# Performance work log

Measured on AMD Instinct MI355X. Metric: run time of the kernel, lower is better.

Reference implementation:

```python
import jax, jax.numpy as jnp
import numpy as np

EMBED_DIM = 1024
NUM_HEADS = 16
HEAD_DIM = EMBED_DIM // NUM_HEADS
SEG_LEN = 1024  # all segment_lengths equal, dilation_rate == 1


def setup_inputs() -> dict:
    key = jax.random.key(0)
    k1, k2, k3 = jax.random.split(key, 3)
    B, S, E = 2, 4096, EMBED_DIM
    x = jax.random.normal(k1, (B, S, E), dtype=jnp.float32)
    w_qkv = jax.random.normal(k2, (3 * E, E), dtype=jnp.float32) * (E ** -0.5)
    b_qkv = jnp.zeros((3 * E,), dtype=jnp.float32)
    w_out = jax.random.normal(k3, (E, E), dtype=jnp.float32) * (E ** -0.5)
    b_out = jnp.zeros((E,), dtype=jnp.float32)
    return {"x": x, "w_qkv": w_qkv, "b_qkv": b_qkv, "w_out": w_out, "b_out": b_out}


def reference(x, w_qkv, b_qkv, w_out, b_out):
    B, S, E = x.shape
    H, Dh = NUM_HEADS, HEAD_DIM
    scale = 1.0 / np.sqrt(Dh).astype(np.float32)
    # QKV projection
    qkv = x @ w_qkv.T + b_qkv                      # [B, S, 3E]
    qkv = qkv.reshape(B, S, 3, H, Dh).transpose(2, 0, 3, 1, 4)  # [3, B, H, S, Dh]
    q, k, v = qkv[0], qkv[1], qkv[2]
    # Segments tile the sequence; each query attends only within its segment
    # (block-diagonal attention; online-softmax combine across segments is
    # trivial since the segments are disjoint in the query dimension).
    n = S // SEG_LEN
    q = q.reshape(B, H, n, SEG_LEN, Dh)
    k = k.reshape(B, H, n, SEG_LEN, Dh)
    v = v.reshape(B, H, n, SEG_LEN, Dh)
    scores = jnp.einsum("bhnqd,bhnkd->bhnqk", q, k) * scale
    attn = jax.nn.softmax(scores, axis=-1)
    out = jnp.einsum("bhnqk,bhnkd->bhnqd", attn, v)  # [B, H, n, seg, Dh]
    out = out.reshape(B, H, S, Dh).transpose(0, 2, 1, 3).reshape(B, S, E)
    return out @ w_out.T + b_out
```

## Files before the change

kernel.cpp:

```cpp
#include <hip/hip_runtime.h>

typedef __bf16 bf16x8 __attribute__((ext_vector_type(8)));
typedef float f32x4 __attribute__((ext_vector_type(4)));

#define SL2E 0.18033688011112042f

__device__ __forceinline__ unsigned short f2bf(float f) {
  union { float f; unsigned u; } v; v.f = f;
  unsigned r = v.u + 0x7fffu + ((v.u >> 16) & 1u);
  return (unsigned short)(r >> 16);
}

__device__ __forceinline__ float fast_exp2(float x) {
#if __has_builtin(__builtin_amdgcn_exp2f)
  return __builtin_amdgcn_exp2f(x);
#else
  return exp2f(x);
#endif
}

__device__ __forceinline__ unsigned pack_bf2(float lo, float hi) {
  union { float f; unsigned u; } a, b;
  a.f = lo; b.f = hi;
#if __has_builtin(__builtin_amdgcn_perm)
  return __builtin_amdgcn_perm(b.u + 0x7fffu, a.u + 0x7fffu, 0x07060302u);
#else
  return ((b.u + 0x7fffu) & 0xffff0000u) | ((a.u + 0x7fffu) >> 16);
#endif
}

__device__ __forceinline__ void gload16(const unsigned short* g, unsigned short* l) {
  __builtin_amdgcn_global_load_lds(
      (const __attribute__((address_space(1))) unsigned int*)g,
      (__attribute__((address_space(3))) unsigned int*)l, 16, 0, 0);
}

#define SWZ(r, cg) ((((r) * 8) + ((cg) ^ ((r) & 7))) * 8)

__global__ __launch_bounds__(256) void f32_to_bf16_all(
    const float* __restrict__ x, const float* __restrict__ wq, const float* __restrict__ wo,
    unsigned short* __restrict__ xb, unsigned short* __restrict__ wqb, unsigned short* __restrict__ wob) {
  int i = blockIdx.x * 256 + threadIdx.x;
  const float* src; unsigned short* dst; int off;
  if (i < 2097152) { src = x; dst = xb; off = i; }
  else if (i < 2883584) { src = wq; dst = wqb; off = i - 2097152; }
  else if (i < 3145728) { src = wo; dst = wob; off = i - 2883584; }
  else return;
  float4 v = ((const float4*)src)[off];
  ushort4 o;
  o.x = f2bf(v.x); o.y = f2bf(v.y); o.z = f2bf(v.z); o.w = f2bf(v.w);
  ((ushort4*)dst)[off] = o;
}


template <bool SWAP>
__device__ __forceinline__ void tile_compute_6x4(
    const unsigned short* As_, const unsigned short* Bs_,
    int l15, int quad, int wm, int wn, f32x4* acc) {
#pragma unroll
  for (int kk = 0; kk < 2; ++kk) {
    int cg = kk * 4 + quad;
    bf16x8 af[4], bfr[6];
#pragma unroll
    for (int i = 0; i < 4; ++i) af[i] = *(const bf16x8*)(As_ + SWZ(wm + i * 16 + l15, cg));
#pragma unroll
    for (int j = 0; j < 6; ++j) bfr[j] = *(const bf16x8*)(Bs_ + SWZ(wn + j * 16 + l15, cg));
    if constexpr (SWAP) {
#pragma unroll
      for (int j = 0; j < 6; ++j)
#pragma unroll
        for (int i = 0; i < 4; ++i)
          acc[j * 4 + i] = __builtin_amdgcn_mfma_f32_16x16x32_bf16(bfr[j], af[i], acc[j * 4 + i], 0, 0, 0);
    } else {
#pragma unroll
      for (int i = 0; i < 4; ++i)
#pragma unroll
        for (int j = 0; j < 6; ++j)
          acc[i * 6 + j] = __builtin_amdgcn_mfma_f32_16x16x32_bf16(af[i], bfr[j], acc[i * 6 + j], 0, 0, 0);
    }
  }
}

template <bool SWAP>
__device__ __forceinline__ void mainloop_256x192(
    const unsigned short* const srcp[7], const int ldso[7],
    unsigned short* lds0, unsigned short* lds1,
    int l15, int quad, int wm, int wn, f32x4* acc) {
#pragma unroll
  for (int i = 0; i < 7; ++i) gload16(srcp[i], lds0 + ldso[i]);
#pragma unroll 1
  for (int t2 = 0; t2 < 16; t2 += 2) {
#pragma unroll
    for (int i = 0; i < 7; ++i) gload16(srcp[i] + (t2 + 1) * 64, lds1 + ldso[i]);
    asm volatile("s_waitcnt vmcnt(7)" ::: "memory");
    __builtin_amdgcn_s_barrier();
    __builtin_amdgcn_sched_barrier(0);
    tile_compute_6x4<SWAP>(lds0, lds0 + 16384, l15, quad, wm, wn, acc);
    __builtin_amdgcn_s_barrier();
    if (t2 < 14) {
#pragma unroll
      for (int i = 0; i < 7; ++i) gload16(srcp[i] + (t2 + 2) * 64, lds0 + ldso[i]);
      asm volatile("s_waitcnt vmcnt(7)" ::: "memory");
    } else {
      asm volatile("s_waitcnt vmcnt(0)" ::: "memory");
    }
    __builtin_amdgcn_s_barrier();
    __builtin_amdgcn_sched_barrier(0);
    tile_compute_6x4<SWAP>(lds1, lds1 + 16384, l15, quad, wm, wn, acc);
    __builtin_amdgcn_s_barrier();
  }
}

__global__ __launch_bounds__(512, 2) void gemm_qkv(
    const unsigned short* __restrict__ A,
    const unsigned short* __restrict__ Bt,
    const float* __restrict__ bias,
    unsigned short* __restrict__ Qb,
    unsigned short* __restrict__ Kb,
    unsigned short* __restrict__ Vtb) {
  const int K = 1024;
  __shared__ unsigned short SMEM[2][28672];
  int tid = threadIdx.x;
  int w = tid >> 6, lane = tid & 63, l15 = lane & 15, quad = lane >> 4;
  int m0 = blockIdx.x * 256, n0 = blockIdx.y * 192;
  int wm = (w & 3) * 64, wn = (w >> 2) * 96;
  int b = m0 >> 12;

  int rlane = lane >> 3;
  int cs = ((lane & 7) ^ rlane) * 8;
  const unsigned short* srcp[7];
  int ldso[7];
#pragma unroll
  for (int i = 0; i < 7; ++i) {
    int q = w * 7 + i;
    if (q < 32) { srcp[i] = A + (m0 + q * 8 + rlane) * K + cs; ldso[i] = q * 512; }
    else { srcp[i] = Bt + (n0 + (q - 32) * 8 + rlane) * K + cs; ldso[i] = 16384 + (q - 32) * 512; }
  }

  f32x4 acc[24] = {};

  bool pureV = (n0 >= 2048);
  bool mixed = (n0 < 2048) && (n0 + 192 > 2048);

  if (!pureV && !mixed) {
    mainloop_256x192<true>(srcp, ldso, &SMEM[0][0], &SMEM[1][0], l15, quad, wm, wn, acc);
    int s_base = (m0 & 4095) + wm;
#pragma unroll
    for (int j = 0; j < 6; ++j) {
      int ng = n0 + wn + j * 16;
      int t = ng >> 10;
      unsigned short* dst = t ? Kb : Qb;
      float sc = t ? 1.0f : SL2E;
      int h = (ng >> 6) & 15;
      int d0 = (ng & 63) + quad * 4;
      float4 bv = *(const float4*)(bias + ng + quad * 4);
      int head_base = (b * 16 + h) * 4096 * 64;
#pragma unroll
      for (int i = 0; i < 4; ++i) {
        int s = s_base + i * 16 + l15;
        f32x4 a = acc[j * 4 + i];
        ushort4 pk;
        pk.x = f2bf((a[0] + bv.x) * sc);
        pk.y = f2bf((a[1] + bv.y) * sc);
        pk.z = f2bf((a[2] + bv.z) * sc);
        pk.w = f2bf((a[3] + bv.w) * sc);
        *(ushort4*)(dst + head_base + s * 64 + d0) = pk;
      }
    }
  } else if (pureV) {
    mainloop_256x192<false>(srcp, ldso, &SMEM[0][0], &SMEM[1][0], l15, quad, wm, wn, acc);
    int sblk = (m0 & 4095) + wm + quad * 4;
#pragma unroll
    for (int j = 0; j < 6; ++j) {
      int n_j = n0 + wn + j * 16 + l15;
      float bv = bias[n_j];
      int h = (n_j >> 6) & 15, d = n_j & 63;
      int vbase = ((b * 16 + h) * 64 + d) * 4096;
#pragma unroll
      for (int i = 0; i < 4; ++i) {
        int s = sblk + i * 16;
        f32x4 a = acc[i * 6 + j];
        ushort4 pk;
        pk.x = f2bf(a[0] + bv);
        pk.y = f2bf(a[1] + bv);
        pk.z = f2bf(a[2] + bv);
        pk.w = f2bf(a[3] + bv);
        *(ushort4*)(Vtb + vbase + s) = pk;
      }
    }
  } else {
    mainloop_256x192<false>(srcp, ldso, &SMEM[0][0], &SMEM[1][0], l15, quad, wm, wn, acc);
#pragma unroll
    for (int j = 0; j < 6; ++j) {
      int ng = n0 + wn + j * 16;
      if (ng >= 2048) {
        int n_j = ng + l15;
        float bv = bias[n_j];
        int h = (n_j >> 6) & 15, d = n_j & 63;
        int vbase = ((b * 16 + h) * 64 + d) * 4096;
        int sblk = (m0 & 4095) + wm + quad * 4;
#pragma unroll
        for (int i = 0; i < 4; ++i) {
          int s = sblk + i * 16;
          f32x4 a = acc[i * 6 + j];
          ushort4 pk;
          pk.x = f2bf(a[0] + bv);
          pk.y = f2bf(a[1] + bv);
          pk.z = f2bf(a[2] + bv);
          pk.w = f2bf(a[3] + bv);
          *(ushort4*)(Vtb + vbase + s) = pk;
        }
      } else {
        int n_j = ng + l15;
        float bv = bias[n_j];
        int h = (n_j >> 6) & 15, d = n_j & 63;
        int kbase = (b * 16 + h) * 4096 * 64 + d;
#pragma unroll
        for (int i = 0; i < 4; ++i) {
          f32x4 a = acc[i * 6 + j];
#pragma unroll
          for (int r = 0; r < 4; ++r) {
            int s = (m0 & 4095) + wm + i * 16 + quad * 4 + r;
            Kb[kbase + s * 64] = f2bf(a[r] + bv);
          }
        }
      }
    }
  }
}

#define LDP 72

__global__ __launch_bounds__(256) void attn_k(
    const unsigned short* __restrict__ Qb,
    const unsigned short* __restrict__ Kb,
    const unsigned short* __restrict__ Vtb,
    unsigned short* __restrict__ Ab) {
  __shared__ unsigned short KV[2][2][4096];
  __shared__ unsigned short Ps[4][16 * LDP];

  int tid = threadIdx.x;
  int idx = blockIdx.x;
  int grp = ((idx >> 5) << 3) | (idx & 7);
  int qblk = (idx >> 3) & 3;
  int seg = grp & 3, h = (grp >> 2) & 15, b = grp >> 6;
  int w = tid >> 6, lane = tid & 63, l15 = lane & 15, quad = lane >> 4;
  int bh = b * 16 + h;
  int q0 = seg * 1024 + qblk * 256 + w * 64;

  const unsigned short* Kg = Kb + (bh * 4096 + seg * 1024) * 64;
  const unsigned short* Vg = Vtb + bh * 64 * 4096 + seg * 1024;

  int r0 = w * 16 + (lane >> 3);
  int cs = ((lane & 7) ^ (lane >> 3)) * 8;

  const unsigned short* Qg = Qb + (bh * 4096 + q0) * 64;
  bf16x8 qf[4][2];
#pragma unroll
  for (int qb = 0; qb < 4; ++qb)
#pragma unroll
    for (int kk = 0; kk < 2; ++kk)
      qf[qb][kk] = *(const bf16x8*)(Qg + (qb * 16 + l15) * 64 + kk * 32 + quad * 8);

  f32x4 o[4][4] = {};
  float lsum[4] = {0.f, 0.f, 0.f, 0.f};
  unsigned short* Pw = Ps[w];

  {
    unsigned short* dk = &KV[0][0][w * 1024];
    unsigned short* dv = &KV[0][1][w * 1024];
    gload16(Kg + r0 * 64 + cs, dk);
    gload16(Kg + (r0 + 8) * 64 + cs, dk + 512);
    gload16(Vg + r0 * 4096 + cs, dv);
    gload16(Vg + (r0 + 8) * 4096 + cs, dv + 512);
  }

#pragma unroll 2
  for (int kt = 0; kt < 16; ++kt) {
    int cur = kt & 1;
    __syncthreads();
    if (kt < 15) {
      unsigned short* dk = &KV[cur ^ 1][0][w * 1024];
      unsigned short* dv = &KV[cur ^ 1][1][w * 1024];
      const unsigned short* kN = Kg + (kt + 1) * 4096;
      const unsigned short* vN = Vg + (kt + 1) * 64;
      gload16(kN + r0 * 64 + cs, dk);
      gload16(kN + (r0 + 8) * 64 + cs, dk + 512);
      gload16(vN + r0 * 4096 + cs, dv);
      gload16(vN + (r0 + 8) * 4096 + cs, dv + 512);
    }
    const unsigned short* Kt = KV[cur][0];
    const unsigned short* Vt = KV[cur][1];

    uint2 pp[4][4];
#pragma unroll
    for (int half = 0; half < 2; ++half) {
      f32x4 st[2][4] = {};
#pragma unroll
      for (int kk = 0; kk < 2; ++kk) {
        int cg = kk * 4 + quad;
        bf16x8 kf0 = *(const bf16x8*)(Kt + SWZ(half * 32 + l15, cg));
        bf16x8 kf1 = *(const bf16x8*)(Kt + SWZ(half * 32 + 16 + l15, cg));
#pragma unroll
        for (int qb = 0; qb < 4; ++qb) {
          st[0][qb] = __builtin_amdgcn_mfma_f32_16x16x32_bf16(kf0, qf[qb][kk], st[0][qb], 0, 0, 0);
          st[1][qb] = __builtin_amdgcn_mfma_f32_16x16x32_bf16(kf1, qf[qb][kk], st[1][qb], 0, 0, 0);
        }
      }
#pragma unroll
      for (int kb = 0; kb < 2; ++kb)
#pragma unroll
        for (int qb = 0; qb < 4; ++qb) {
          f32x4 s = st[kb][qb];
          float p0 = fast_exp2(s[0]), p1 = fast_exp2(s[1]);
          float p2 = fast_exp2(s[2]), p3 = fast_exp2(s[3]);
          lsum[qb] += (p0 + p1) + (p2 + p3);
          uint2 d;
          d.x = pack_bf2(p0, p1);
          d.y = pack_bf2(p2, p3);
          pp[qb][half * 2 + kb] = d;
        }
    }

    bf16x8 vf[2][4];
#pragma unroll
    for (int kk = 0; kk < 2; ++kk)
#pragma unroll
      for (int db = 0; db < 4; ++db)
        vf[kk][db] = *(const bf16x8*)(Vt + SWZ(db * 16 + l15, kk * 4 + quad));
#pragma unroll
    for (int qb = 0; qb < 4; ++qb) {
#pragma unroll
      for (int g = 0; g < 4; ++g)
        *(uint2*)(Pw + l15 * LDP + g * 16 + quad * 4) = pp[qb][g];
#pragma unroll
      for (int kk = 0; kk < 2; ++kk) {
        bf16x8 pa = *(const bf16x8*)(Pw + l15 * LDP + kk * 32 + quad * 8);
#pragma unroll
        for (int db = 0; db < 4; ++db)
          o[qb][db] = __builtin_amdgcn_mfma_f32_16x16x32_bf16(pa, vf[kk][db], o[qb][db], 0, 0, 0);
      }
    }
  }

#pragma unroll
  for (int qb = 0; qb < 4; ++qb) {
    lsum[qb] += __shfl_xor(lsum[qb], 16);
    lsum[qb] += __shfl_xor(lsum[qb], 32);
  }

  float* Wf = (float*)(&KV[0][0][0]) + w * 1024;
#pragma unroll
  for (int qb = 0; qb < 4; ++qb) {
#pragma unroll
    for (int db = 0; db < 4; ++db)
#pragma unroll
      for (int r = 0; r < 4; ++r)
        Wf[(quad * 4 + r) * 64 + db * 16 + l15] = o[qb][db][r];
    float inv = 1.0f / lsum[qb];
    float4 x0 = *(float4*)(Wf + l15 * 64 + quad * 8);
    float4 x1 = *(float4*)(Wf + l15 * 64 + quad * 8 + 4);
    float4 x2 = *(float4*)(Wf + l15 * 64 + (quad + 4) * 8);
    float4 x3 = *(float4*)(Wf + l15 * 64 + (quad + 4) * 8 + 4);
    uint4 u0, u1;
    u0.x = pack_bf2(x0.x * inv, x0.y * inv);
    u0.y = pack_bf2(x0.z * inv, x0.w * inv);
    u0.z = pack_bf2(x1.x * inv, x1.y * inv);
    u0.w = pack_bf2(x1.z * inv, x1.w * inv);
    u1.x = pack_bf2(x2.x * inv, x2.y * inv);
    u1.y = pack_bf2(x2.z * inv, x2.w * inv);
    u1.z = pack_bf2(x3.x * inv, x3.y * inv);
    u1.w = pack_bf2(x3.z * inv, x3.w * inv);
    int sg = q0 + qb * 16 + l15;
    int base = (b * 4096 + sg) * 1024 + h * 64;
    *(uint4*)(Ab + base + quad * 8) = u0;
    *(uint4*)(Ab + base + (quad + 4) * 8) = u1;
  }
}

__global__ __launch_bounds__(256) void gemm_out(
    const unsigned short* __restrict__ A,
    const unsigned short* __restrict__ Bt,
    const float* __restrict__ bias,
    float* __restrict__ C) {
  const int K = 1024;
  __shared__ unsigned short As2[2][8192];
  __shared__ unsigned short Bs2[2][8192];
  int tid = threadIdx.x;
  int m0 = blockIdx.x * 128, n0 = blockIdx.y * 128;
  int w = tid >> 6, lane = tid & 63, l15 = lane & 15, quad = lane >> 4;
  int wm = (w & 1) * 64, wn = (w >> 1) * 64;

  f32x4 acc[4][4] = {};

  int rs = w * 32 + (lane >> 3);
  int cs = ((lane & 7) ^ (lane >> 3)) * 8;
  const unsigned short* Ag = A + (m0 + rs) * K + cs;
  const unsigned short* Bg = Bt + (n0 + rs) * K + cs;

#pragma unroll
  for (int i = 0; i < 4; ++i) {
    gload16(Ag + i * 8 * K, &As2[0][0] + w * 2048 + i * 512);
    gload16(Bg + i * 8 * K, &Bs2[0][0] + w * 2048 + i * 512);
  }
#pragma unroll 1
  for (int kt2 = 0; kt2 < 16; kt2 += 2) {
#pragma unroll
    for (int half = 0; half < 2; ++half) {
      int kt = kt2 + half;
      unsigned short* Awr = half ? &As2[0][0] : &As2[1][0];
      unsigned short* Bwr = half ? &Bs2[0][0] : &Bs2[1][0];
      const unsigned short* Ard = half ? &As2[1][0] : &As2[0][0];
      const unsigned short* Brd = half ? &Bs2[1][0] : &Bs2[0][0];
      if (kt < 15) {
#pragma unroll
        for (int i = 0; i < 4; ++i) {
          gload16(Ag + i * 8 * K + (kt + 1) * 64, Awr + w * 2048 + i * 512);
          gload16(Bg + i * 8 * K + (kt + 1) * 64, Bwr + w * 2048 + i * 512);
        }
        asm volatile("s_waitcnt vmcnt(8)" ::: "memory");
      } else {
        asm volatile("s_waitcnt vmcnt(0)" ::: "memory");
      }
      __builtin_amdgcn_s_barrier();
      __builtin_amdgcn_sched_barrier(0);
#pragma unroll
      for (int kk = 0; kk < 2; ++kk) {
        int swk = (((kk * 4 + quad) ^ (l15 & 7))) * 8;
        bf16x8 af[4], bfr[4];
#pragma unroll
        for (int i = 0; i < 4; ++i) af[i] = *(const bf16x8*)(Ard + (wm + i * 16 + l15) * 64 + swk);
#pragma unroll
        for (int j = 0; j < 4; ++j) bfr[j] = *(const bf16x8*)(Brd + (wn + j * 16 + l15) * 64 + swk);
#pragma unroll
        for (int j = 0; j < 4; ++j)
#pragma unroll
          for (int i = 0; i < 4; ++i)
            acc[j][i] = __builtin_amdgcn_mfma_f32_16x16x32_bf16(bfr[j], af[i], acc[j][i], 0, 0, 0);
      }
      __builtin_amdgcn_s_barrier();
    }
  }

#pragma unroll
  for (int j = 0; j < 4; ++j) {
    int nb = n0 + wn + j * 16 + quad * 4;
    float4 bv = *(const float4*)(bias + nb);
#pragma unroll
    for (int i = 0; i < 4; ++i) {
      int m = m0 + wm + i * 16 + l15;
      float4 ov;
      ov.x = acc[j][i][0] + bv.x;
      ov.y = acc[j][i][1] + bv.y;
      ov.z = acc[j][i][2] + bv.z;
      ov.w = acc[j][i][3] + bv.w;
      *(float4*)(C + m * 1024 + nb) = ov;
    }
  }
}

extern "C" void kernel_launch(void* const* d_in, const int* in_sizes, int n_in,
                              void* d_out, int out_size, void* d_ws, size_t ws_size,
                              hipStream_t stream) {
  const float* x     = (const float*)d_in[0];
  const float* w_qkv = (const float*)d_in[1];
  const float* b_qkv = (const float*)d_in[2];
  const float* w_out = (const float*)d_in[3];
  const float* b_out = (const float*)d_in[4];
  float* out = (float*)d_out;
  char* ws = (char*)d_ws;

  unsigned short* wqkvb = (unsigned short*)(ws);
  unsigned short* woutb = (unsigned short*)(ws + 6291456);
  unsigned short* Qb    = (unsigned short*)(ws + 8388608);
  unsigned short* Kb    = (unsigned short*)(ws + 25165824);
  unsigned short* Vtb   = (unsigned short*)(ws + 41943040);
  unsigned short* xb    = (unsigned short*)(ws + 58720256);
  unsigned short* Ab    = xb;

  f32_to_bf16_all<<<12288, 256, 0, stream>>>(x, w_qkv, w_out, xb, wqkvb, woutb);
  gemm_qkv<<<dim3(32, 16), 512, 0, stream>>>(xb, wqkvb, b_qkv, Qb, Kb, Vtb);
  attn_k<<<512, 256, 0, stream>>>(Qb, Kb, Vtb, Ab);
  gemm_out<<<dim3(64, 8), 256, 0, stream>>>(Ab, woutb, b_out, out);
}
```

Baseline: 231.3 us.

## Split GEMM tile compute into four phases interleaving global prefetch with MFMA

Restructures the 256x192 GEMM mainloop so each K-tile compute is split into four phases. Each phase issues LDS fragment reads and a slice of the next tile's global-to-LDS loads, syncs, then runs 12 MFMAs under raised wave priority. The intent is to spread memory traffic across the compute and keep the matrix units fed, in the style of ping-pong scheduling. The cost is more barriers per tile and a full vmcnt(0) wait before each tile, which removes the earlier deeper prefetch slack.

```diff
diff --git a/kernel.cpp b/kernel.cpp
--- a/kernel.cpp
+++ b/kernel.cpp
@@ -54,31 +54,68 @@
 
 
 template <bool SWAP>
-__device__ __forceinline__ void tile_compute_6x4(
-    const unsigned short* As_, const unsigned short* Bs_,
+__device__ __forceinline__ void mfma12(f32x4* acc, bf16x8 af0, bf16x8 af1,
+                                       const bf16x8 bfr[6], int ib) {
+#pragma unroll
+  for (int j = 0; j < 6; ++j) {
+    if constexpr (SWAP) {
+      acc[j * 4 + ib]     = __builtin_amdgcn_mfma_f32_16x16x32_bf16(bfr[j], af0, acc[j * 4 + ib], 0, 0, 0);
+      acc[j * 4 + ib + 1] = __builtin_amdgcn_mfma_f32_16x16x32_bf16(bfr[j], af1, acc[j * 4 + ib + 1], 0, 0, 0);
+    } else {
+      acc[ib * 6 + j]       = __builtin_amdgcn_mfma_f32_16x16x32_bf16(af0, bfr[j], acc[ib * 6 + j], 0, 0, 0);
+      acc[(ib + 1) * 6 + j] = __builtin_amdgcn_mfma_f32_16x16x32_bf16(af1, bfr[j], acc[(ib + 1) * 6 + j], 0, 0, 0);
+    }
+  }
+}
+
+#define PH_SYNC() do { \
+    __builtin_amdgcn_s_barrier(); \
+    asm volatile("s_waitcnt lgkmcnt(0)" ::: "memory"); \
+    __builtin_amdgcn_sched_barrier(0); \
+  } while (0)
+
+template <bool SWAP>
+__device__ __forceinline__ void tile_4ph(
+    const unsigned short* R, unsigned short* W,
+    const unsigned short* const srcp[7], const int ldso[7], int koff, bool do_stage,
     int l15, int quad, int wm, int wn, f32x4* acc) {
-#pragma unroll
-  for (int kk = 0; kk < 2; ++kk) {
-    int cg = kk * 4 + quad;
-    bf16x8 af[4], bfr[6];
-#pragma unroll
-    for (int i = 0; i < 4; ++i) af[i] = *(const bf16x8*)(As_ + SWZ(wm + i * 16 + l15, cg));
-#pragma unroll
-    for (int j = 0; j < 6; ++j) bfr[j] = *(const bf16x8*)(Bs_ + SWZ(wn + j * 16 + l15, cg));
-    if constexpr (SWAP) {
-#pragma unroll
-      for (int j = 0; j < 6; ++j)
-#pragma unroll
-        for (int i = 0; i < 4; ++i)
-          acc[j * 4 + i] = __builtin_amdgcn_mfma_f32_16x16x32_bf16(bfr[j], af[i], acc[j * 4 + i], 0, 0, 0);
-    } else {
-#pragma unroll
-      for (int i = 0; i < 4; ++i)
-#pragma unroll
-        for (int j = 0; j < 6; ++j)
-          acc[i * 6 + j] = __builtin_amdgcn_mfma_f32_16x16x32_bf16(af[i], bfr[j], acc[i * 6 + j], 0, 0, 0);
-    }
-  }
+  const unsigned short* Bs_ = R + 16384;
+  bf16x8 af0, af1, bfr[6];
+  af0 = *(const bf16x8*)(R + SWZ(wm + l15, quad));
+  af1 = *(const bf16x8*)(R + SWZ(wm + 16 + l15, quad));
+#pragma unroll
+  for (int j = 0; j < 6; ++j) bfr[j] = *(const bf16x8*)(Bs_ + SWZ(wn + j * 16 + l15, quad));
+  if (do_stage) { gload16(srcp[0] + koff, W + ldso[0]); gload16(srcp[1] + koff, W + ldso[1]); }
+  PH_SYNC();
+  __builtin_amdgcn_s_setprio(1);
+  mfma12<SWAP>(acc, af0, af1, bfr, 0);
+  __builtin_amdgcn_s_setprio(0);
+  __builtin_amdgcn_s_barrier();
+  af0 = *(const bf16x8*)(R + SWZ(wm + 32 + l15, quad));
+  af1 = *(const bf16x8*)(R + SWZ(wm + 48 + l15, quad));
+  if (do_stage) { gload16(srcp[2] + koff, W + ldso[2]); gload16(srcp[3] + koff, W + ldso[3]); }
+  PH_SYNC();
+  __builtin_amdgcn_s_setprio(1);
+  mfma12<SWAP>(acc, af0, af1, bfr, 2);
+  __builtin_amdgcn_s_setprio(0);
+  __builtin_amdgcn_s_barrier();
+  af0 = *(const bf16x8*)(R + SWZ(wm + l15, 4 + quad));
+  af1 = *(const bf16x8*)(R + SWZ(wm + 16 + l15, 4 + quad));
+#pragma unroll
+  for (int j = 0; j < 6; ++j) bfr[j] = *(const bf16x8*)(Bs_ + SWZ(wn + j * 16 + l15, 4 + quad));
+  if (do_stage) { gload16(srcp[4] + koff, W + ldso[4]); gload16(srcp[5] + koff, W + ldso[5]); }
+  PH_SYNC();
+  __builtin_amdgcn_s_setprio(1);
+  mfma12<SWAP>(acc, af0, af1, bfr, 0);
+  __builtin_amdgcn_s_setprio(0);
+  __builtin_amdgcn_s_barrier();
+  af0 = *(const bf16x8*)(R + SWZ(wm + 32 + l15, 4 + quad));
+  af1 = *(const bf16x8*)(R + SWZ(wm + 48 + l15, 4 + quad));
+  if (do_stage) { gload16(srcp[6] + koff, W + ldso[6]); }
+  PH_SYNC();
+  __builtin_amdgcn_s_setprio(1);
+  mfma12<SWAP>(acc, af0, af1, bfr, 2);
+  __builtin_amdgcn_s_setprio(0);
 }
 
 template <bool SWAP>
@@ -90,24 +127,12 @@
   for (int i = 0; i < 7; ++i) gload16(srcp[i], lds0 + ldso[i]);
 #pragma unroll 1
   for (int t2 = 0; t2 < 16; t2 += 2) {
-#pragma unroll
-    for (int i = 0; i < 7; ++i) gload16(srcp[i] + (t2 + 1) * 64, lds1 + ldso[i]);
-    asm volatile("s_waitcnt vmcnt(7)" ::: "memory");
+    asm volatile("s_waitcnt vmcnt(0)" ::: "memory");
     __builtin_amdgcn_s_barrier();
-    __builtin_amdgcn_sched_barrier(0);
-    tile_compute_6x4<SWAP>(lds0, lds0 + 16384, l15, quad, wm, wn, acc);
+    tile_4ph<SWAP>(lds0, lds1, srcp, ldso, (t2 + 1) * 64, true, l15, quad, wm, wn, acc);
+    asm volatile("s_waitcnt vmcnt(0)" ::: "memory");
     __builtin_amdgcn_s_barrier();
-    if (t2 < 14) {
-#pragma unroll
-      for (int i = 0; i < 7; ++i) gload16(srcp[i] + (t2 + 2) * 64, lds0 + ldso[i]);
-      asm volatile("s_waitcnt vmcnt(7)" ::: "memory");
-    } else {
-      asm volatile("s_waitcnt vmcnt(0)" ::: "memory");
-    }
-    __builtin_amdgcn_s_barrier();
-    __builtin_amdgcn_sched_barrier(0);
-    tile_compute_6x4<SWAP>(lds1, lds1 + 16384, l15, quad, wm, wn, acc);
-    __builtin_amdgcn_s_barrier();
+    tile_4ph<SWAP>(lds1, lds0, srcp, ldso, (t2 + 2) * 64, t2 < 14, l15, quad, wm, wn, acc);
   }
 }
 
```

Measured after the change: 230.8 us. No clear change (-0.2%).

## Split attention block across 8 waves with 32 queries per wave

Applied to the files above, without the earlier changes.

The attention kernel now launches 512 threads per block (8 waves), each wave handling 32 query rows instead of 64. Each wave issues one K and one V cooperative load per tile instead of two, which halves per-wave register state (o, qf, pp) and raises occupancy via launch_bounds(512,4). The P staging buffer grows to hold 32 rows per wave, and a barrier is added before reusing the KV shared memory for the output transpose. The trade-off is that each K/V tile loaded into LDS now feeds fewer queries per wave, so MFMA work per LDS fragment read drops.

```diff
diff --git a/kernel.cpp b/kernel.cpp
--- a/kernel.cpp
+++ b/kernel.cpp
@@ -231,13 +231,13 @@
 
 #define LDP 72
 
-__global__ __launch_bounds__(256) void attn_k(
+__global__ __launch_bounds__(512, 4) void attn_k(
     const unsigned short* __restrict__ Qb,
     const unsigned short* __restrict__ Kb,
     const unsigned short* __restrict__ Vtb,
     unsigned short* __restrict__ Ab) {
   __shared__ unsigned short KV[2][2][4096];
-  __shared__ unsigned short Ps[4][16 * LDP];
+  __shared__ unsigned short Ps[8][32 * LDP];
 
   int tid = threadIdx.x;
   int idx = blockIdx.x;
@@ -246,63 +246,52 @@
   int seg = grp & 3, h = (grp >> 2) & 15, b = grp >> 6;
   int w = tid >> 6, lane = tid & 63, l15 = lane & 15, quad = lane >> 4;
   int bh = b * 16 + h;
-  int q0 = seg * 1024 + qblk * 256 + w * 64;
+  int q0 = seg * 1024 + qblk * 256 + w * 32;
 
   const unsigned short* Kg = Kb + (bh * 4096 + seg * 1024) * 64;
   const unsigned short* Vg = Vtb + bh * 64 * 4096 + seg * 1024;
 
-  int r0 = w * 16 + (lane >> 3);
-  int cs = ((lane & 7) ^ (lane >> 3)) * 8;
+  int rlane = lane >> 3;
+  int cs = ((lane & 7) ^ rlane) * 8;
+  int srow = w * 8 + rlane;
 
   const unsigned short* Qg = Qb + (bh * 4096 + q0) * 64;
-  bf16x8 qf[4][2];
-#pragma unroll
-  for (int qb = 0; qb < 4; ++qb)
+  bf16x8 qf[2][2];
+#pragma unroll
+  for (int qb = 0; qb < 2; ++qb)
 #pragma unroll
     for (int kk = 0; kk < 2; ++kk)
       qf[qb][kk] = *(const bf16x8*)(Qg + (qb * 16 + l15) * 64 + kk * 32 + quad * 8);
 
-  f32x4 o[4][4] = {};
-  float lsum[4] = {0.f, 0.f, 0.f, 0.f};
+  f32x4 o[2][4] = {};
+  float lsum[2] = {0.f, 0.f};
   unsigned short* Pw = Ps[w];
 
-  {
-    unsigned short* dk = &KV[0][0][w * 1024];
-    unsigned short* dv = &KV[0][1][w * 1024];
-    gload16(Kg + r0 * 64 + cs, dk);
-    gload16(Kg + (r0 + 8) * 64 + cs, dk + 512);
-    gload16(Vg + r0 * 4096 + cs, dv);
-    gload16(Vg + (r0 + 8) * 4096 + cs, dv + 512);
-  }
+  gload16(Kg + srow * 64 + cs, &KV[0][0][w * 512]);
+  gload16(Vg + srow * 4096 + cs, &KV[0][1][w * 512]);
 
 #pragma unroll 2
   for (int kt = 0; kt < 16; ++kt) {
     int cur = kt & 1;
     __syncthreads();
     if (kt < 15) {
-      unsigned short* dk = &KV[cur ^ 1][0][w * 1024];
-      unsigned short* dv = &KV[cur ^ 1][1][w * 1024];
-      const unsigned short* kN = Kg + (kt + 1) * 4096;
-      const unsigned short* vN = Vg + (kt + 1) * 64;
-      gload16(kN + r0 * 64 + cs, dk);
-      gload16(kN + (r0 + 8) * 64 + cs, dk + 512);
-      gload16(vN + r0 * 4096 + cs, dv);
-      gload16(vN + (r0 + 8) * 4096 + cs, dv + 512);
+      gload16(Kg + (kt + 1) * 4096 + srow * 64 + cs, &KV[cur ^ 1][0][w * 512]);
+      gload16(Vg + (kt + 1) * 64 + srow * 4096 + cs, &KV[cur ^ 1][1][w * 512]);
     }
     const unsigned short* Kt = KV[cur][0];
     const unsigned short* Vt = KV[cur][1];
 
-    uint2 pp[4][4];
+    uint2 pp[2][4];
 #pragma unroll
     for (int half = 0; half < 2; ++half) {
-      f32x4 st[2][4] = {};
+      f32x4 st[2][2] = {};
 #pragma unroll
       for (int kk = 0; kk < 2; ++kk) {
         int cg = kk * 4 + quad;
         bf16x8 kf0 = *(const bf16x8*)(Kt + SWZ(half * 32 + l15, cg));
         bf16x8 kf1 = *(const bf16x8*)(Kt + SWZ(half * 32 + 16 + l15, cg));
 #pragma unroll
-        for (int qb = 0; qb < 4; ++qb) {
+        for (int qb = 0; qb < 2; ++qb) {
           st[0][qb] = __builtin_amdgcn_mfma_f32_16x16x32_bf16(kf0, qf[qb][kk], st[0][qb], 0, 0, 0);
           st[1][qb] = __builtin_amdgcn_mfma_f32_16x16x32_bf16(kf1, qf[qb][kk], st[1][qb], 0, 0, 0);
         }
@@ -310,7 +299,7 @@
 #pragma unroll
       for (int kb = 0; kb < 2; ++kb)
 #pragma unroll
-        for (int qb = 0; qb < 4; ++qb) {
+        for (int qb = 0; qb < 2; ++qb) {
           f32x4 s = st[kb][qb];
           float p0 = fast_exp2(s[0]), p1 = fast_exp2(s[1]);
           float p2 = fast_exp2(s[2]), p3 = fast_exp2(s[3]);
@@ -322,36 +311,38 @@
         }
     }
 
-    bf16x8 vf[2][4];
-#pragma unroll
-    for (int kk = 0; kk < 2; ++kk)
+#pragma unroll
+    for (int qb = 0; qb < 2; ++qb)
+#pragma unroll
+      for (int g = 0; g < 4; ++g)
+        *(uint2*)(Pw + qb * 16 * LDP + l15 * LDP + g * 16 + quad * 4) = pp[qb][g];
+
+#pragma unroll
+    for (int kk = 0; kk < 2; ++kk) {
+      bf16x8 vfk[4];
 #pragma unroll
       for (int db = 0; db < 4; ++db)
-        vf[kk][db] = *(const bf16x8*)(Vt + SWZ(db * 16 + l15, kk * 4 + quad));
-#pragma unroll
-    for (int qb = 0; qb < 4; ++qb) {
-#pragma unroll
-      for (int g = 0; g < 4; ++g)
-        *(uint2*)(Pw + l15 * LDP + g * 16 + quad * 4) = pp[qb][g];
-#pragma unroll
-      for (int kk = 0; kk < 2; ++kk) {
-        bf16x8 pa = *(const bf16x8*)(Pw + l15 * LDP + kk * 32 + quad * 8);
+        vfk[db] = *(const bf16x8*)(Vt + SWZ(db * 16 + l15, kk * 4 + quad));
+#pragma unroll
+      for (int qb = 0; qb < 2; ++qb) {
+        bf16x8 pa = *(const bf16x8*)(Pw + qb * 16 * LDP + l15 * LDP + kk * 32 + quad * 8);
 #pragma unroll
         for (int db = 0; db < 4; ++db)
-          o[qb][db] = __builtin_amdgcn_mfma_f32_16x16x32_bf16(pa, vf[kk][db], o[qb][db], 0, 0, 0);
-      }
-    }
-  }
-
-#pragma unroll
-  for (int qb = 0; qb < 4; ++qb) {
+          o[qb][db] = __builtin_amdgcn_mfma_f32_16x16x32_bf16(pa, vfk[db], o[qb][db], 0, 0, 0);
+      }
+    }
+  }
+
+#pragma unroll
+  for (int qb = 0; qb < 2; ++qb) {
     lsum[qb] += __shfl_xor(lsum[qb], 16);
     lsum[qb] += __shfl_xor(lsum[qb], 32);
   }
 
+  __syncthreads();
   float* Wf = (float*)(&KV[0][0][0]) + w * 1024;
 #pragma unroll
-  for (int qb = 0; qb < 4; ++qb) {
+  for (int qb = 0; qb < 2; ++qb) {
 #pragma unroll
     for (int db = 0; db < 4; ++db)
 #pragma unroll
@@ -480,6 +471,6 @@
 
   f32_to_bf16_all<<<12288, 256, 0, stream>>>(x, w_qkv, w_out, xb, wqkvb, woutb);
   gemm_qkv<<<dim3(32, 16), 512, 0, stream>>>(xb, wqkvb, b_qkv, Qb, Kb, Vtb);
-  attn_k<<<512, 256, 0, stream>>>(Qb, Kb, Vtb, Ab);
+  attn_k<<<512, 512, 0, stream>>>(Qb, Kb, Vtb, Ab);
   gemm_out<<<dim3(64, 8), 256, 0, stream>>>(Ab, woutb, b_out, out);
 }
```

New measurement: 227.2 us. About the same (-1.8%).
